# Kernel optimization log

Measured on AMD Instinct MI355X. Metric: run time of the kernel, lower is better.

## Reference

```python
import jax, jax.numpy as jnp
import numpy as np

K_DIM = 1024
HEADS = 16
D_K = K_DIM // HEADS


def setup_inputs() -> dict:
    key = jax.random.key(0)
    ks = jax.random.split(key, 6)
    b, t, k = 4, 1024, K_DIM
    scale = 1.0 / np.sqrt(k)
    return {
        "x": jax.random.normal(ks[0], (b, t, k), dtype=jnp.float32),
        "Wq": jax.random.normal(ks[1], (k, k), dtype=jnp.float32) * scale,
        "Wk": jax.random.normal(ks[2], (k, k), dtype=jnp.float32) * scale,
        "Wv": jax.random.normal(ks[3], (k, k), dtype=jnp.float32) * scale,
        "Wo": jax.random.normal(ks[4], (k, k), dtype=jnp.float32) * scale,
        "bo": jax.random.normal(ks[5], (k,), dtype=jnp.float32) * 0.01,
    }


def reference(x, Wq, Wk, Wv, Wo, bo):
    b, t, k = x.shape
    h, d_k = HEADS, D_K
    # Linear(k,k) applies x @ W.T; project then split heads -> [b, h, t, d_k]
    Q = (x @ Wq.T).reshape(b, t, h, d_k).transpose(0, 2, 1, 3)
    Kh = (x @ Wk.T).reshape(b, t, h, d_k).transpose(0, 2, 1, 3)
    V = (x @ Wv.T).reshape(b, t, h, d_k).transpose(0, 2, 1, 3)
    scores = jnp.einsum("bhqd,bhkd->bhqk", Q, Kh) / jnp.sqrt(jnp.float32(d_k))
    attn = jax.nn.softmax(scores, axis=-1)
    out = jnp.einsum("bhqk,bhkd->bhqd", attn, V)
    out = out.transpose(0, 2, 1, 3).reshape(b, t, k)
    return out @ Wo.T + bo
```

## Files before the change

kernel.cpp:

```cpp
#include <hip/hip_runtime.h>
#include <hip/hip_bf16.h>

typedef __attribute__((ext_vector_type(4))) float f32x4;
typedef __attribute__((ext_vector_type(8))) short short8;

#define B_   4
#define T_   1024
#define H_   16
#define DK_  64
#define KDIM 1024

#define QSCALE 0.18033688011112042f

__device__ __forceinline__ unsigned short f2bf(float f){
  union { float f; unsigned int u; } a; a.f = f;
  unsigned int u = a.u;
  return (unsigned short)((u + 0x7FFFu + ((u >> 16) & 1u)) >> 16);
}

__device__ __forceinline__ unsigned short f2bf_rn(float f){
  union { __hip_bfloat16 h; unsigned short u; } cv;
  cv.h = __float2bfloat16(f);
  return cv.u;
}

__device__ __forceinline__ void gload16(const void* g, void* l){
  __builtin_amdgcn_global_load_lds(
      (const __attribute__((address_space(1))) unsigned int*)g,
      (__attribute__((address_space(3))) unsigned int*)l,
      16, 0, 0);
}

__global__ __launch_bounds__(256) void convert5(
    const float* __restrict__ x,  const float* __restrict__ wq,
    const float* __restrict__ wk, const float* __restrict__ wv,
    const float* __restrict__ wo,
    short* __restrict__ xb,  short* __restrict__ wqb,
    short* __restrict__ wkb, short* __restrict__ wvb, short* __restrict__ wob)
{
  int i = blockIdx.x * 256 + threadIdx.x;
  const float* s; short* d; int off;
  if (i < (1 << 20)) { s = x; d = xb; off = i; }
  else {
    int j = i - (1 << 20);
    int w = j >> 18;
    off = j & ((1 << 18) - 1);
    s = (w == 0) ? wq : (w == 1) ? wk : (w == 2) ? wv : wo;
    d = (w == 0) ? wqb : (w == 1) ? wkb : (w == 2) ? wvb : wob;
  }
  float4 v = ((const float4*)s)[off];
  ushort4 o;
  o.x = f2bf(v.x); o.y = f2bf(v.y); o.z = f2bf(v.z); o.w = f2bf(v.w);
  ((ushort4*)d)[off] = o;
}

__device__ __forceinline__ void gemm_core(const short* __restrict__ A,
                                          const short* __restrict__ W,
                                          int m0, int n0,
                                          short* Als, short* Bls,
                                          f32x4 acc[4][4])
{
  const int tid = threadIdx.x;
  const int wv = tid >> 6, lane = tid & 63;
  const int lr = lane & 15, lq = lane >> 4;
  const int wr = wv >> 1, wc = wv & 1;
#pragma unroll
  for (int m = 0; m < 4; ++m)
#pragma unroll
    for (int n = 0; n < 4; ++n) acc[m][n] = (f32x4){0.f, 0.f, 0.f, 0.f};

  const int r0 = tid >> 2;
  const int c0 = (tid & 3) * 8;

  auto stage = [&](int buf, int ks) {
    const int k0 = ks * 32;
#pragma unroll
    for (int p = 0; p < 2; ++p) {
      const int r = p * 64 + r0;
      const short* ga = A + (size_t)(m0 + r) * KDIM + k0 + c0;
      const short* gb = W + (size_t)(n0 + r) * KDIM + k0 + c0;
      short* la = Als + buf * 4096 + p * 2048 + wv * 512;
      short* lb = Bls + buf * 4096 + p * 2048 + wv * 512;
      gload16(ga, la);
      gload16(gb, lb);
    }
  };

  stage(0, 0);
  __syncthreads();
  for (int ks = 0; ks < 32; ++ks) {
    const int cur = ks & 1;
    if (ks + 1 < 32) stage(cur ^ 1, ks + 1);
    const short* Ab = Als + cur * 4096;
    const short* Bb = Bls + cur * 4096;
    short8 af[4], bfr[4];
#pragma unroll
    for (int i = 0; i < 4; ++i) {
      af[i]  = *(const short8*)(Ab + (wr * 64 + i * 16 + lr) * 32 + lq * 8);
      bfr[i] = *(const short8*)(Bb + (wc * 64 + i * 16 + lr) * 32 + lq * 8);
    }
#pragma unroll
    for (int m = 0; m < 4; ++m)
#pragma unroll
      for (int n = 0; n < 4; ++n)
        acc[m][n] = __builtin_amdgcn_mfma_f32_16x16x32_bf16(af[m], bfr[n], acc[m][n], 0, 0, 0);
    __syncthreads();
  }
}

__global__ __launch_bounds__(256, 2) void gemm_qkv(
    const short* __restrict__ xb,
    const short* __restrict__ Wqb, const short* __restrict__ Wkb, const short* __restrict__ Wvb,
    short* __restrict__ Qb, short* __restrict__ Kb, short* __restrict__ VTb)
{
  __shared__ short Als[2 * 4096];
  __shared__ short Bls[2 * 4096];
  const int m0 = blockIdx.x * 128;
  const int by = blockIdx.y;
  const int wsel = by >> 3;
  const int n0 = (by & 7) * 128;
  const short* W = (wsel == 0) ? Wqb : (wsel == 1) ? Wkb : Wvb;
  f32x4 acc[4][4];
  gemm_core(xb, W, m0, n0, Als, Bls, acc);

  const int tid = threadIdx.x, lane = tid & 63, wv = tid >> 6;
  const int lr = lane & 15, lq = lane >> 4, wr = wv >> 1, wc = wv & 1;
  if (wsel < 2) {
    short* O = wsel ? Kb : Qb;
    const float sc = wsel ? 1.0f : QSCALE;
#pragma unroll
    for (int m = 0; m < 4; ++m)
#pragma unroll
      for (int n = 0; n < 4; ++n)
#pragma unroll
        for (int j = 0; j < 4; ++j) {
          int row = m0 + wr * 64 + m * 16 + lq * 4 + j;
          int col = n0 + wc * 64 + n * 16 + lr;
          O[(size_t)row * KDIM + col] = (short)f2bf(acc[m][n][j] * sc);
        }
  } else {
#pragma unroll
    for (int m = 0; m < 4; ++m)
#pragma unroll
      for (int n = 0; n < 4; ++n) {
        int row = m0 + wr * 64 + m * 16 + lq * 4;
        int col = n0 + wc * 64 + n * 16 + lr;
        int b = row >> 10, t = row & 1023, h = col >> 6, d = col & 63;
        ushort4 v;
        v.x = f2bf(acc[m][n][0]); v.y = f2bf(acc[m][n][1]);
        v.z = f2bf(acc[m][n][2]); v.w = f2bf(acc[m][n][3]);
        *(ushort4*)&VTb[(size_t)((b * 16 + h) * 64 + d) * 1024 + t] = v;
      }
  }
}

__global__ __launch_bounds__(256) void attn_kern(
    const short* __restrict__ Qb, const short* __restrict__ Kb,
    const short* __restrict__ VTb, short* __restrict__ AOb)
{
  __shared__ __align__(16) short kl[2][128 * 64];
  __shared__ __align__(16) short vl[2][64 * 128];
  __shared__ __align__(16) short pl[4][16 * 64];
  const int bh = blockIdx.y, b = bh >> 4, h = bh & 15;
  const int q0 = blockIdx.x * 64;
  const int tid = threadIdx.x, wv = tid >> 6, lane = tid & 63;
  const int lr = lane & 15, lq = lane >> 4;

  const short* Qrow = Qb + (size_t)(b * T_ + q0 + wv * 16 + lr) * KDIM + h * DK_;
  short8 qf0 = *(const short8*)(Qrow + lq * 8);
  short8 qf1 = *(const short8*)(Qrow + 32 + lq * 8);

  const short* Kbase = Kb + (size_t)(b * T_) * KDIM + h * DK_;
  const short* Vbase = VTb + (size_t)(bh * DK_) * 1024;

  const int krow_ = tid >> 3, kcol_ = (tid & 7) * 8;
  const int vrow_ = tid >> 4, vcol_ = (tid & 15) * 8;

  auto stage = [&](int buf, int kv0) {
#pragma unroll
    for (int p = 0; p < 4; ++p) {
      const int r = p * 32 + krow_;
      gload16(Kbase + (size_t)(kv0 + r) * KDIM + (kcol_ ^ ((r & 7) << 3)),
              &kl[buf][p * 2048 + wv * 512]);
    }
#pragma unroll
    for (int p = 0; p < 4; ++p) {
      const int r = p * 16 + vrow_;
      gload16(Vbase + (size_t)r * 1024 + kv0 + (vcol_ ^ ((r & 7) << 3)),
              &vl[buf][p * 2048 + wv * 512]);
    }
  };

  f32x4 oacc[4];
#pragma unroll
  for (int i = 0; i < 4; ++i) oacc[i] = (f32x4){0.f, 0.f, 0.f, 0.f};
  float m_r = -1e30f, l_r = 0.f;
  const int swq = (lr & 7) << 3;
  short* plw = pl[wv];

  int cur = 0;
  stage(0, 0);
  __syncthreads();

  for (int kt = 0; kt < 16384 / (128 * 1024 / T_); ++kt) { }

  for (int kt = 0; kt < 8; ++kt) {
    if (kt < 7) stage(cur ^ 1, (kt + 1) * 128);

    f32x4 s[8];
#pragma unroll
    for (int nt = 0; nt < 8; ++nt) {
      const int kr = nt * 16 + lr;
      const int sw = (kr & 7) << 3;
      short8 kf0 = *(const short8*)&kl[cur][kr * 64 + ((lq * 8) ^ sw)];
      short8 kf1 = *(const short8*)&kl[cur][kr * 64 + ((32 + lq * 8) ^ sw)];
      f32x4 z = (f32x4){0.f, 0.f, 0.f, 0.f};
      z = __builtin_amdgcn_mfma_f32_16x16x32_bf16(kf0, qf0, z, 0, 0, 0);
      s[nt] = __builtin_amdgcn_mfma_f32_16x16x32_bf16(kf1, qf1, z, 0, 0, 0);
    }

    float t0, t1, mx;
    {
      float a0 = fmaxf(fmaxf(s[0][0], s[0][1]), fmaxf(s[0][2], s[0][3]));
      float a1 = fmaxf(fmaxf(s[1][0], s[1][1]), fmaxf(s[1][2], s[1][3]));
      float a2 = fmaxf(fmaxf(s[2][0], s[2][1]), fmaxf(s[2][2], s[2][3]));
      float a3 = fmaxf(fmaxf(s[3][0], s[3][1]), fmaxf(s[3][2], s[3][3]));
      float a4 = fmaxf(fmaxf(s[4][0], s[4][1]), fmaxf(s[4][2], s[4][3]));
      float a5 = fmaxf(fmaxf(s[5][0], s[5][1]), fmaxf(s[5][2], s[5][3]));
      float a6 = fmaxf(fmaxf(s[6][0], s[6][1]), fmaxf(s[6][2], s[6][3]));
      float a7 = fmaxf(fmaxf(s[7][0], s[7][1]), fmaxf(s[7][2], s[7][3]));
      t0 = fmaxf(fmaxf(a0, a1), fmaxf(a2, a3));
      t1 = fmaxf(fmaxf(a4, a5), fmaxf(a6, a7));
      mx = fmaxf(t0, t1);
    }
    mx = fmaxf(mx, __shfl_xor(mx, 16));
    mx = fmaxf(mx, __shfl_xor(mx, 32));
    if (!__all(mx <= m_r + 8.f)) {
      const float mn = fmaxf(m_r, mx);
      const float al = exp2f(m_r - mn);
      l_r *= al;
#pragma unroll
      for (int nt = 0; nt < 4; ++nt)
#pragma unroll
        for (int j = 0; j < 4; ++j) oacc[nt][j] *= al;
      m_r = mn;
    }
    float rs = 0.f;
#pragma unroll
    for (int nt = 0; nt < 8; ++nt)
#pragma unroll
      for (int j = 0; j < 4; ++j) {
        float e = exp2f(s[nt][j] - m_r);
        s[nt][j] = e;
        rs += e;
      }
    rs += __shfl_xor(rs, 16);
    rs += __shfl_xor(rs, 32);
    l_r += rs;

#pragma unroll
    for (int half = 0; half < 2; ++half) {
#pragma unroll
      for (int nt = 0; nt < 4; ++nt) {
        f32x4 v = s[half * 4 + nt];
        ushort4 u;
        u.x = f2bf_rn(v[0]); u.y = f2bf_rn(v[1]);
        u.z = f2bf_rn(v[2]); u.w = f2bf_rn(v[3]);
        *(ushort4*)&plw[lr * 64 + ((nt * 16 + lq * 4) ^ swq)] = u;
      }
      asm volatile("s_waitcnt lgkmcnt(0)" ::: "memory");
      short8 pf0 = *(const short8*)&plw[lr * 64 + ((lq * 8) ^ swq)];
      short8 pf1 = *(const short8*)&plw[lr * 64 + ((32 + lq * 8) ^ swq)];
#pragma unroll
      for (int ntd = 0; ntd < 4; ++ntd) {
        const int vr = ntd * 16 + lr;
        const int sw = (vr & 7) << 3;
        short8 vf0 = *(const short8*)&vl[cur][vr * 128 + ((half * 64 + lq * 8) ^ sw)];
        short8 vf1 = *(const short8*)&vl[cur][vr * 128 + ((half * 64 + 32 + lq * 8) ^ sw)];
        oacc[ntd] = __builtin_amdgcn_mfma_f32_16x16x32_bf16(vf0, pf0, oacc[ntd], 0, 0, 0);
        oacc[ntd] = __builtin_amdgcn_mfma_f32_16x16x32_bf16(vf1, pf1, oacc[ntd], 0, 0, 0);
      }
    }
    __syncthreads();
    cur ^= 1;
  }

  const float inv = 1.0f / l_r;
#pragma unroll
  for (int nt = 0; nt < 4; ++nt) {
    ushort4 u;
    u.x = f2bf_rn(oacc[nt][0] * inv);
    u.y = f2bf_rn(oacc[nt][1] * inv);
    u.z = f2bf_rn(oacc[nt][2] * inv);
    u.w = f2bf_rn(oacc[nt][3] * inv);
    *(ushort4*)&AOb[(size_t)(b * T_ + q0 + wv * 16 + lr) * KDIM + h * DK_ + nt * 16 + lq * 4] = u;
  }
}

__global__ __launch_bounds__(256, 2) void gemm_out(
    const short* __restrict__ AOb, const short* __restrict__ Wob,
    const float* __restrict__ bias, float* __restrict__ out)
{
  __shared__ short Als[2 * 4096];
  __shared__ short Bls[2 * 4096];
  const int m0 = blockIdx.x * 128;
  const int n0 = blockIdx.y * 128;
  f32x4 acc[4][4];
  gemm_core(AOb, Wob, m0, n0, Als, Bls, acc);

  const int tid = threadIdx.x, lane = tid & 63, wv = tid >> 6;
  const int lr = lane & 15, lq = lane >> 4, wr = wv >> 1, wc = wv & 1;
#pragma unroll
  for (int m = 0; m < 4; ++m)
#pragma unroll
    for (int n = 0; n < 4; ++n) {
      int col = n0 + wc * 64 + n * 16 + lr;
      float bv = bias[col];
#pragma unroll
      for (int j = 0; j < 4; ++j) {
        int row = m0 + wr * 64 + m * 16 + lq * 4 + j;
        out[(size_t)row * KDIM + col] = acc[m][n][j] + bv;
      }
    }
}

extern "C" void kernel_launch(void* const* d_in, const int* in_sizes, int n_in,
                              void* d_out, int out_size, void* d_ws, size_t ws_size,
                              hipStream_t stream) {
  const float* x  = (const float*)d_in[0];
  const float* Wq = (const float*)d_in[1];
  const float* Wk = (const float*)d_in[2];
  const float* Wv = (const float*)d_in[3];
  const float* Wo = (const float*)d_in[4];
  const float* bo = (const float*)d_in[5];

  short* ws = (short*)d_ws;
  short* xb  = ws;
  short* Wqb = ws + 4194304;
  short* Wkb = ws + 5242880;
  short* Wvb = ws + 6291456;
  short* Wob = ws + 7340032;
  short* Qb  = ws + 8388608;
  short* Kb  = ws + 12582912;
  short* VTb = ws + 16777216;
  short* AOb = ws + 20971520;

  convert5<<<8192, 256, 0, stream>>>(x, Wq, Wk, Wv, Wo, xb, Wqb, Wkb, Wvb, Wob);
  gemm_qkv<<<dim3(32, 24), 256, 0, stream>>>(xb, Wqb, Wkb, Wvb, Qb, Kb, VTb);
  attn_kern<<<dim3(16, 64), 256, 0, stream>>>(Qb, Kb, VTb, AOb);
  gemm_out<<<dim3(32, 8), 256, 0, stream>>>(AOb, Wob, bo, (float*)d_out);
}
```

Before: 186.1 us.

## Use triple-buffered 8-wave GEMMs with XCD-aware block remap; shrink attention KV tile

Both projection GEMMs now use a shared 512-thread core with 64-wide K steps and three LDS buffers. It manages explicit vmcnt waits, staggers its prefetches between MFMA phases and raises priority with setprio. Block ids are remapped so neighbouring tiles land on the same XCD. The QKV GEMM grows its M tile to 256. The attention kernel drops from 128 to 64 keys per tile, which halves LDS use and register pressure but doubles loop iterations. The large LDS footprint (about 144KB for QKV) may limit residency to one block per CU.

```diff
diff --git a/kernel.cpp b/kernel.cpp
--- a/kernel.cpp
+++ b/kernel.cpp
@@ -29,6 +29,12 @@
       (const __attribute__((address_space(1))) unsigned int*)g,
       (__attribute__((address_space(3))) unsigned int*)l,
       16, 0, 0);
+}
+
+template<int N> __device__ __forceinline__ void wait_vmcnt(){
+  if constexpr (N == 0)      asm volatile("s_waitcnt vmcnt(0)" ::: "memory");
+  else if constexpr (N == 4) asm volatile("s_waitcnt vmcnt(4)" ::: "memory");
+  else if constexpr (N == 6) asm volatile("s_waitcnt vmcnt(6)" ::: "memory");
 }
 
 __global__ __launch_bounds__(256) void convert5(
@@ -54,77 +60,106 @@
   ((ushort4*)d)[off] = o;
 }
 
-__device__ __forceinline__ void gemm_core(const short* __restrict__ A,
-                                          const short* __restrict__ W,
-                                          int m0, int n0,
-                                          short* Als, short* Bls,
-                                          f32x4 acc[4][4])
-{
+template<int BM, int BN>
+__device__ __forceinline__ void stage_range(
+    const short* __restrict__ A, const short* __restrict__ W,
+    int m0, int n0, int kt, int lo, int hi,
+    short* Asb, short* Bsb, int wv, int lane)
+{
+  constexpr int LA = BM / 64, LB = BN / 64;
+  const int r8 = lane >> 3, c8 = (lane & 7) * 8;
+#pragma unroll
+  for (int i = lo; i < hi; ++i) {
+    if (i < LA) {
+      const int r = (wv * LA + i) * 8 + r8;
+      gload16(A + (size_t)(m0 + r) * KDIM + kt * 64 + c8, Asb + (wv * LA + i) * 512);
+    } else {
+      const int ib = i - LA;
+      const int r = (wv * LB + ib) * 8 + r8;
+      gload16(W + (size_t)(n0 + r) * KDIM + kt * 64 + c8, Bsb + (wv * LB + ib) * 512);
+    }
+  }
+}
+
+template<int BM, int BN>
+__device__ __forceinline__ void gemm8_core(
+    const short* __restrict__ A, const short* __restrict__ W,
+    int m0, int n0, short* As, short* Bs,
+    f32x4 acc[BM / 64][BN / 32])
+{
+  constexpr int M_REP = BM / 64, N_REP = BN / 32;
+  constexpr int LA = BM / 64, LB = BN / 64, L = LA + LB;
+  constexpr int NKT = 16;
   const int tid = threadIdx.x;
   const int wv = tid >> 6, lane = tid & 63;
   const int lr = lane & 15, lq = lane >> 4;
-  const int wr = wv >> 1, wc = wv & 1;
-#pragma unroll
-  for (int m = 0; m < 4; ++m)
-#pragma unroll
-    for (int n = 0; n < 4; ++n) acc[m][n] = (f32x4){0.f, 0.f, 0.f, 0.f};
-
-  const int r0 = tid >> 2;
-  const int c0 = (tid & 3) * 8;
-
-  auto stage = [&](int buf, int ks) {
-    const int k0 = ks * 32;
-#pragma unroll
-    for (int p = 0; p < 2; ++p) {
-      const int r = p * 64 + r0;
-      const short* ga = A + (size_t)(m0 + r) * KDIM + k0 + c0;
-      const short* gb = W + (size_t)(n0 + r) * KDIM + k0 + c0;
-      short* la = Als + buf * 4096 + p * 2048 + wv * 512;
-      short* lb = Bls + buf * 4096 + p * 2048 + wv * 512;
-      gload16(ga, la);
-      gload16(gb, lb);
-    }
-  };
-
-  stage(0, 0);
-  __syncthreads();
-  for (int ks = 0; ks < 32; ++ks) {
-    const int cur = ks & 1;
-    if (ks + 1 < 32) stage(cur ^ 1, ks + 1);
-    const short* Ab = Als + cur * 4096;
-    const short* Bb = Bls + cur * 4096;
-    short8 af[4], bfr[4];
-#pragma unroll
-    for (int i = 0; i < 4; ++i) {
-      af[i]  = *(const short8*)(Ab + (wr * 64 + i * 16 + lr) * 32 + lq * 8);
-      bfr[i] = *(const short8*)(Bb + (wc * 64 + i * 16 + lr) * 32 + lq * 8);
-    }
-#pragma unroll
-    for (int m = 0; m < 4; ++m)
-#pragma unroll
-      for (int n = 0; n < 4; ++n)
-        acc[m][n] = __builtin_amdgcn_mfma_f32_16x16x32_bf16(af[m], bfr[n], acc[m][n], 0, 0, 0);
-    __syncthreads();
-  }
-}
-
-__global__ __launch_bounds__(256, 2) void gemm_qkv(
+  const int wm = wv >> 1, wn = wv & 1;
+  const int arow = wm * (BM / 4);
+  const int brow = wn * (BN / 2);
+
+#pragma unroll
+  for (int m = 0; m < M_REP; ++m)
+#pragma unroll
+    for (int n = 0; n < N_REP; ++n) acc[m][n] = (f32x4){0.f, 0.f, 0.f, 0.f};
+
+  stage_range<BM, BN>(A, W, m0, n0, 0, 0, L, As,             Bs,             wv, lane);
+  stage_range<BM, BN>(A, W, m0, n0, 1, 0, L, As + BM * 64,   Bs + BN * 64,   wv, lane);
+
+  int buf = 0;
+  for (int kt = 0; kt < NKT; ++kt) {
+    if (kt < NKT - 1) wait_vmcnt<L>(); else wait_vmcnt<0>();
+    __builtin_amdgcn_s_barrier();
+    const short* Ab = As + buf * (BM * 64);
+    const short* Bb = Bs + buf * (BN * 64);
+    const int sb = (buf >= 1) ? buf - 1 : 2;
+    short* Asb = As + sb * (BM * 64);
+    short* Bsb = Bs + sb * (BN * 64);
+#pragma unroll
+    for (int kk = 0; kk < 2; ++kk) {
+      short8 af[M_REP], bfv[N_REP];
+#pragma unroll
+      for (int m = 0; m < M_REP; ++m)
+        af[m] = *(const short8*)(Ab + (arow + m * 16 + lr) * 64 + kk * 32 + lq * 8);
+#pragma unroll
+      for (int n = 0; n < N_REP; ++n)
+        bfv[n] = *(const short8*)(Bb + (brow + n * 16 + lr) * 64 + kk * 32 + lq * 8);
+      if (kt + 2 < NKT)
+        stage_range<BM, BN>(A, W, m0, n0, kt + 2, kk * (L / 2), (kk + 1) * (L / 2),
+                            Asb, Bsb, wv, lane);
+      __builtin_amdgcn_s_barrier();
+      __builtin_amdgcn_s_setprio(1);
+#pragma unroll
+      for (int m = 0; m < M_REP; ++m)
+#pragma unroll
+        for (int n = 0; n < N_REP; ++n)
+          acc[m][n] = __builtin_amdgcn_mfma_f32_16x16x32_bf16(af[m], bfv[n], acc[m][n], 0, 0, 0);
+      __builtin_amdgcn_s_setprio(0);
+      __builtin_amdgcn_sched_barrier(0);
+      __builtin_amdgcn_s_barrier();
+    }
+    buf = (buf == 2) ? 0 : buf + 1;
+  }
+}
+
+__global__ __launch_bounds__(512, 2) void gemm8_qkv(
     const short* __restrict__ xb,
     const short* __restrict__ Wqb, const short* __restrict__ Wkb, const short* __restrict__ Wvb,
     short* __restrict__ Qb, short* __restrict__ Kb, short* __restrict__ VTb)
 {
-  __shared__ short Als[2 * 4096];
-  __shared__ short Bls[2 * 4096];
-  const int m0 = blockIdx.x * 128;
-  const int by = blockIdx.y;
-  const int wsel = by >> 3;
-  const int n0 = (by & 7) * 128;
+  __shared__ __align__(16) short As[3 * 256 * 64];
+  __shared__ __align__(16) short Bs[3 * 128 * 64];
+  const int bid = blockIdx.x;
+  const int wgid = (bid & 7) * 48 + (bid >> 3);
+  const int mx = wgid & 15, nyy = wgid >> 4;
+  const int wsel = nyy >> 3;
+  const int m0 = mx * 256, n0 = (nyy & 7) * 128;
   const short* W = (wsel == 0) ? Wqb : (wsel == 1) ? Wkb : Wvb;
+
   f32x4 acc[4][4];
-  gemm_core(xb, W, m0, n0, Als, Bls, acc);
+  gemm8_core<256, 128>(xb, W, m0, n0, As, Bs, acc);
 
   const int tid = threadIdx.x, lane = tid & 63, wv = tid >> 6;
-  const int lr = lane & 15, lq = lane >> 4, wr = wv >> 1, wc = wv & 1;
+  const int lr = lane & 15, lq = lane >> 4, wm = wv >> 1, wn = wv & 1;
   if (wsel < 2) {
     short* O = wsel ? Kb : Qb;
     const float sc = wsel ? 1.0f : QSCALE;
@@ -134,8 +169,8 @@
       for (int n = 0; n < 4; ++n)
 #pragma unroll
         for (int j = 0; j < 4; ++j) {
-          int row = m0 + wr * 64 + m * 16 + lq * 4 + j;
-          int col = n0 + wc * 64 + n * 16 + lr;
+          int row = m0 + wm * 64 + m * 16 + lq * 4 + j;
+          int col = n0 + wn * 64 + n * 16 + lr;
           O[(size_t)row * KDIM + col] = (short)f2bf(acc[m][n][j] * sc);
         }
   } else {
@@ -143,8 +178,8 @@
     for (int m = 0; m < 4; ++m)
 #pragma unroll
       for (int n = 0; n < 4; ++n) {
-        int row = m0 + wr * 64 + m * 16 + lq * 4;
-        int col = n0 + wc * 64 + n * 16 + lr;
+        int row = m0 + wm * 64 + m * 16 + lq * 4;
+        int col = n0 + wn * 64 + n * 16 + lr;
         int b = row >> 10, t = row & 1023, h = col >> 6, d = col & 63;
         ushort4 v;
         v.x = f2bf(acc[m][n][0]); v.y = f2bf(acc[m][n][1]);
@@ -154,12 +189,42 @@
   }
 }
 
+__global__ __launch_bounds__(512, 2) void gemm8_out(
+    const short* __restrict__ AOb, const short* __restrict__ Wob,
+    const float* __restrict__ bias, float* __restrict__ out)
+{
+  __shared__ __align__(16) short As[3 * 128 * 64];
+  __shared__ __align__(16) short Bs[3 * 128 * 64];
+  const int bid = blockIdx.x;
+  const int wgid = (bid & 7) * 32 + (bid >> 3);
+  const int mx = wgid & 31, ny = wgid >> 5;
+  const int m0 = mx * 128, n0 = ny * 128;
+
+  f32x4 acc[2][4];
+  gemm8_core<128, 128>(AOb, Wob, m0, n0, As, Bs, acc);
+
+  const int tid = threadIdx.x, lane = tid & 63, wv = tid >> 6;
+  const int lr = lane & 15, lq = lane >> 4, wm = wv >> 1, wn = wv & 1;
+#pragma unroll
+  for (int m = 0; m < 2; ++m)
+#pragma unroll
+    for (int n = 0; n < 4; ++n) {
+      int col = n0 + wn * 64 + n * 16 + lr;
+      float bv = bias[col];
+#pragma unroll
+      for (int j = 0; j < 4; ++j) {
+        int row = m0 + wm * 32 + m * 16 + lq * 4 + j;
+        out[(size_t)row * KDIM + col] = acc[m][n][j] + bv;
+      }
+    }
+}
+
 __global__ __launch_bounds__(256) void attn_kern(
     const short* __restrict__ Qb, const short* __restrict__ Kb,
     const short* __restrict__ VTb, short* __restrict__ AOb)
 {
-  __shared__ __align__(16) short kl[2][128 * 64];
-  __shared__ __align__(16) short vl[2][64 * 128];
+  __shared__ __align__(16) short kl[2][64 * 64];
+  __shared__ __align__(16) short vl[2][64 * 64];
   __shared__ __align__(16) short pl[4][16 * 64];
   const int bh = blockIdx.y, b = bh >> 4, h = bh & 15;
   const int q0 = blockIdx.x * 64;
@@ -173,20 +238,19 @@
   const short* Kbase = Kb + (size_t)(b * T_) * KDIM + h * DK_;
   const short* Vbase = VTb + (size_t)(bh * DK_) * 1024;
 
-  const int krow_ = tid >> 3, kcol_ = (tid & 7) * 8;
-  const int vrow_ = tid >> 4, vcol_ = (tid & 15) * 8;
+  const int srow = tid >> 3, scol = (tid & 7) * 8;
 
   auto stage = [&](int buf, int kv0) {
 #pragma unroll
-    for (int p = 0; p < 4; ++p) {
-      const int r = p * 32 + krow_;
-      gload16(Kbase + (size_t)(kv0 + r) * KDIM + (kcol_ ^ ((r & 7) << 3)),
+    for (int p = 0; p < 2; ++p) {
+      const int r = p * 32 + srow;
+      gload16(Kbase + (size_t)(kv0 + r) * KDIM + (scol ^ ((r & 7) << 3)),
               &kl[buf][p * 2048 + wv * 512]);
     }
 #pragma unroll
-    for (int p = 0; p < 4; ++p) {
-      const int r = p * 16 + vrow_;
-      gload16(Vbase + (size_t)r * 1024 + kv0 + (vcol_ ^ ((r & 7) << 3)),
+    for (int p = 0; p < 2; ++p) {
+      const int r = p * 32 + srow;
+      gload16(Vbase + (size_t)r * 1024 + kv0 + (scol ^ ((r & 7) << 3)),
               &vl[buf][p * 2048 + wv * 512]);
     }
   };
@@ -202,36 +266,28 @@
   stage(0, 0);
   __syncthreads();
 
-  for (int kt = 0; kt < 16384 / (128 * 1024 / T_); ++kt) { }
-
-  for (int kt = 0; kt < 8; ++kt) {
-    if (kt < 7) stage(cur ^ 1, (kt + 1) * 128);
-
-    f32x4 s[8];
-#pragma unroll
-    for (int nt = 0; nt < 8; ++nt) {
+  for (int kt = 0; kt < 16; ++kt) {
+    if (kt < 15) stage(cur ^ 1, (kt + 1) * 64);
+
+    f32x4 s[4];
+#pragma unroll
+    for (int nt = 0; nt < 4; ++nt) {
       const int kr = nt * 16 + lr;
       const int sw = (kr & 7) << 3;
       short8 kf0 = *(const short8*)&kl[cur][kr * 64 + ((lq * 8) ^ sw)];
       short8 kf1 = *(const short8*)&kl[cur][kr * 64 + ((32 + lq * 8) ^ sw)];
       f32x4 z = (f32x4){0.f, 0.f, 0.f, 0.f};
       z = __builtin_amdgcn_mfma_f32_16x16x32_bf16(kf0, qf0, z, 0, 0, 0);
-      s[nt] = __builtin_amdgcn_mfma_f32_16x16x32_bf16(kf1, qf1, z, 0, 0, 0);
-    }
-
-    float t0, t1, mx;
+      s[nt] = __builtin_amdgcn_mfma_f32_16x16x32_bf16(kf1, qf1, s[nt] = z, 0, 0, 0);
+    }
+
+    float mx;
     {
       float a0 = fmaxf(fmaxf(s[0][0], s[0][1]), fmaxf(s[0][2], s[0][3]));
       float a1 = fmaxf(fmaxf(s[1][0], s[1][1]), fmaxf(s[1][2], s[1][3]));
       float a2 = fmaxf(fmaxf(s[2][0], s[2][1]), fmaxf(s[2][2], s[2][3]));
       float a3 = fmaxf(fmaxf(s[3][0], s[3][1]), fmaxf(s[3][2], s[3][3]));
-      float a4 = fmaxf(fmaxf(s[4][0], s[4][1]), fmaxf(s[4][2], s[4][3]));
-      float a5 = fmaxf(fmaxf(s[5][0], s[5][1]), fmaxf(s[5][2], s[5][3]));
-      float a6 = fmaxf(fmaxf(s[6][0], s[6][1]), fmaxf(s[6][2], s[6][3]));
-      float a7 = fmaxf(fmaxf(s[7][0], s[7][1]), fmaxf(s[7][2], s[7][3]));
-      t0 = fmaxf(fmaxf(a0, a1), fmaxf(a2, a3));
-      t1 = fmaxf(fmaxf(a4, a5), fmaxf(a6, a7));
-      mx = fmaxf(t0, t1);
+      mx = fmaxf(fmaxf(a0, a1), fmaxf(a2, a3));
     }
     mx = fmaxf(mx, __shfl_xor(mx, 16));
     mx = fmaxf(mx, __shfl_xor(mx, 32));
@@ -247,7 +303,7 @@
     }
     float rs = 0.f;
 #pragma unroll
-    for (int nt = 0; nt < 8; ++nt)
+    for (int nt = 0; nt < 4; ++nt)
 #pragma unroll
       for (int j = 0; j < 4; ++j) {
         float e = exp2f(s[nt][j] - m_r);
@@ -259,27 +315,24 @@
     l_r += rs;
 
 #pragma unroll
-    for (int half = 0; half < 2; ++half) {
-#pragma unroll
-      for (int nt = 0; nt < 4; ++nt) {
-        f32x4 v = s[half * 4 + nt];
-        ushort4 u;
-        u.x = f2bf_rn(v[0]); u.y = f2bf_rn(v[1]);
-        u.z = f2bf_rn(v[2]); u.w = f2bf_rn(v[3]);
-        *(ushort4*)&plw[lr * 64 + ((nt * 16 + lq * 4) ^ swq)] = u;
-      }
-      asm volatile("s_waitcnt lgkmcnt(0)" ::: "memory");
-      short8 pf0 = *(const short8*)&plw[lr * 64 + ((lq * 8) ^ swq)];
-      short8 pf1 = *(const short8*)&plw[lr * 64 + ((32 + lq * 8) ^ swq)];
-#pragma unroll
-      for (int ntd = 0; ntd < 4; ++ntd) {
-        const int vr = ntd * 16 + lr;
-        const int sw = (vr & 7) << 3;
-        short8 vf0 = *(const short8*)&vl[cur][vr * 128 + ((half * 64 + lq * 8) ^ sw)];
-        short8 vf1 = *(const short8*)&vl[cur][vr * 128 + ((half * 64 + 32 + lq * 8) ^ sw)];
-        oacc[ntd] = __builtin_amdgcn_mfma_f32_16x16x32_bf16(vf0, pf0, oacc[ntd], 0, 0, 0);
-        oacc[ntd] = __builtin_amdgcn_mfma_f32_16x16x32_bf16(vf1, pf1, oacc[ntd], 0, 0, 0);
-      }
+    for (int nt = 0; nt < 4; ++nt) {
+      f32x4 v = s[nt];
+      ushort4 u;
+      u.x = f2bf_rn(v[0]); u.y = f2bf_rn(v[1]);
+      u.z = f2bf_rn(v[2]); u.w = f2bf_rn(v[3]);
+      *(ushort4*)&plw[lr * 64 + ((nt * 16 + lq * 4) ^ swq)] = u;
+    }
+    asm volatile("s_waitcnt lgkmcnt(0)" ::: "memory");
+    short8 pf0 = *(const short8*)&plw[lr * 64 + ((lq * 8) ^ swq)];
+    short8 pf1 = *(const short8*)&plw[lr * 64 + ((32 + lq * 8) ^ swq)];
+#pragma unroll
+    for (int ntd = 0; ntd < 4; ++ntd) {
+      const int vr = ntd * 16 + lr;
+      const int sw = (vr & 7) << 3;
+      short8 vf0 = *(const short8*)&vl[cur][vr * 64 + ((lq * 8) ^ sw)];
+      short8 vf1 = *(const short8*)&vl[cur][vr * 64 + ((32 + lq * 8) ^ sw)];
+      oacc[ntd] = __builtin_amdgcn_mfma_f32_16x16x32_bf16(vf0, pf0, oacc[ntd], 0, 0, 0);
+      oacc[ntd] = __builtin_amdgcn_mfma_f32_16x16x32_bf16(vf1, pf1, oacc[ntd], 0, 0, 0);
     }
     __syncthreads();
     cur ^= 1;
@@ -295,33 +348,6 @@
     u.w = f2bf_rn(oacc[nt][3] * inv);
     *(ushort4*)&AOb[(size_t)(b * T_ + q0 + wv * 16 + lr) * KDIM + h * DK_ + nt * 16 + lq * 4] = u;
   }
-}
-
-__global__ __launch_bounds__(256, 2) void gemm_out(
-    const short* __restrict__ AOb, const short* __restrict__ Wob,
-    const float* __restrict__ bias, float* __restrict__ out)
-{
-  __shared__ short Als[2 * 4096];
-  __shared__ short Bls[2 * 4096];
-  const int m0 = blockIdx.x * 128;
-  const int n0 = blockIdx.y * 128;
-  f32x4 acc[4][4];
-  gemm_core(AOb, Wob, m0, n0, Als, Bls, acc);
-
-  const int tid = threadIdx.x, lane = tid & 63, wv = tid >> 6;
-  const int lr = lane & 15, lq = lane >> 4, wr = wv >> 1, wc = wv & 1;
-#pragma unroll
-  for (int m = 0; m < 4; ++m)
-#pragma unroll
-    for (int n = 0; n < 4; ++n) {
-      int col = n0 + wc * 64 + n * 16 + lr;
-      float bv = bias[col];
-#pragma unroll
-      for (int j = 0; j < 4; ++j) {
-        int row = m0 + wr * 64 + m * 16 + lq * 4 + j;
-        out[(size_t)row * KDIM + col] = acc[m][n][j] + bv;
-      }
-    }
 }
 
 extern "C" void kernel_launch(void* const* d_in, const int* in_sizes, int n_in,
@@ -346,7 +372,7 @@
   short* AOb = ws + 20971520;
 
   convert5<<<8192, 256, 0, stream>>>(x, Wq, Wk, Wv, Wo, xb, Wqb, Wkb, Wvb, Wob);
-  gemm_qkv<<<dim3(32, 24), 256, 0, stream>>>(xb, Wqb, Wkb, Wvb, Qb, Kb, VTb);
+  gemm8_qkv<<<384, 512, 0, stream>>>(xb, Wqb, Wkb, Wvb, Qb, Kb, VTb);
   attn_kern<<<dim3(16, 64), 256, 0, stream>>>(Qb, Kb, VTb, AOb);
-  gemm_out<<<dim3(32, 8), 256, 0, stream>>>(AOb, Wob, bo, (float*)d_out);
-}
+  gemm8_out<<<256, 512, 0, stream>>>(AOb, Wob, bo, (float*)d_out);
+}
```

Result: slower. 203.3 us (+9.3%).
